# Optimization experiments

Measured on AMD Instinct MI355X. Metric: run time of the kernel, lower is better.

## Reference

```python
import jax, jax.numpy as jnp
import numpy as np

T, B, M, K, N = 8, 1, 16384, 128, 1024


def setup_inputs() -> dict:
    key = jax.random.key(0)
    k1, k2, k3 = jax.random.split(key, 3)
    inputs = jax.random.normal(k1, (T, B, M, K), dtype=jnp.float32)
    weights = jax.random.normal(k2, (T, B, K, N), dtype=jnp.float32) * (1.0 / np.sqrt(K))
    biases = jax.random.normal(k3, (T, 1, 1, N), dtype=jnp.float32)
    return {"inputs": inputs, "weights": weights, "biases": biases}


def reference(inputs, weights, biases):
    # FusedCombineBmm.forward with 3D per-group inputs:
    #   stack -> bmm over T*B -> view [T,B,M,N] -> + stacked bias -> gelu
    # inputs: [T,B,M,K], weights: [T,B,K,N], biases: [T,1,1,N]
    out = jnp.einsum('tbmk,tbkn->tbmn', inputs, weights)
    out = out + biases  # broadcast per-expert bias over (B, M)
    # act == 'gelu' (exact erf form, matching torch's default gelu)
    return jax.nn.gelu(out, approximate=False)
```

## Files before the change

kernel.cpp:

```cpp
#include <hip/hip_runtime.h>

#define T_DIM 8
#define M_DIM 16384
#define K_DIM 128
#define N_DIM 1024

typedef __attribute__((ext_vector_type(8))) short bf16x8_t;
typedef __attribute__((ext_vector_type(4))) float f32x4_t;

__device__ __forceinline__ unsigned short f2bf(float f) {
  unsigned int v;
  __builtin_memcpy(&v, &f, 4);
  v += 0x7FFFu + ((v >> 16) & 1u);
  return (unsigned short)(v >> 16);
}

__device__ __forceinline__ float gelu_tanh(float x) {
  float xc = fminf(fmaxf(x, -8.f), 8.f);
  float y = 2.3022144f * __builtin_fmaf(0.044715f * xc * xc, xc, xc);
  float t = __builtin_amdgcn_exp2f(y);
  return x * t * __builtin_amdgcn_rcpf(t + 1.0f);
}

__global__ __launch_bounds__(256) void transpose_w(
    const float* __restrict__ W, unsigned short* __restrict__ WT) {
  __shared__ __align__(16) unsigned short tile[64][72];
  int b = blockIdx.x;
  int t = b >> 5;
  int r = b & 31;
  int kt = r >> 4;
  int nt = r & 15;
  int tid = threadIdx.x;
  const float* src =
      W + (size_t)t * (K_DIM * N_DIM) + (size_t)(kt * 64) * N_DIM + nt * 64;
#pragma unroll
  for (int it = 0; it < 4; ++it) {
    int li = it * 256 + tid;
    int k = li >> 4;
    int c = li & 15;
    float4 v = *(const float4*)(src + (size_t)k * N_DIM + c * 4);
    unsigned short u[4] = {f2bf(v.x), f2bf(v.y), f2bf(v.z), f2bf(v.w)};
    *(uint2*)&tile[k][c * 4] = *(const uint2*)u;
  }
  __syncthreads();
  unsigned short* dst =
      WT + (size_t)t * (N_DIM * K_DIM) + (size_t)(nt * 64) * K_DIM + kt * 64;
#pragma unroll
  for (int it = 0; it < 2; ++it) {
    int li = it * 256 + tid;
    int n = li >> 3;
    int ck = li & 7;
    __align__(16) unsigned short tmp[8];
#pragma unroll
    for (int j = 0; j < 8; ++j) tmp[j] = tile[ck * 8 + j][n];
    *(uint4*)(dst + (size_t)n * K_DIM + ck * 8) = *(const uint4*)tmp;
  }
}

__global__ __launch_bounds__(256, 3) void gemm_bias_gelu(
    const float* __restrict__ A,
    const unsigned short* __restrict__ WT,
    const float* __restrict__ bias,
    float* __restrict__ O) {
  constexpr int BM = 64;
  constexpr int LDT = 136;
  __shared__ __align__(16) unsigned short sA[BM * LDT];

  int bid = blockIdx.x;
  int t = bid >> 8;
  int mt = bid & 255;
  int tid = threadIdx.x;
  int lane = tid & 63;
  int wn = tid >> 6;
  int qk = lane >> 4;
  int lr = lane & 15;

  const float* Ag =
      A + (size_t)t * ((size_t)M_DIM * K_DIM) + (size_t)(mt * BM) * K_DIM;
#pragma unroll
  for (int it = 0; it < 8; ++it) {
    int li = it * 256 + tid;
    int row = li >> 5;
    int c = li & 31;
    float4 va = *(const float4*)(Ag + (size_t)row * K_DIM + c * 4);
    unsigned short u[4] = {f2bf(va.x), f2bf(va.y), f2bf(va.z), f2bf(va.w)};
    *(uint2*)&sA[row * LDT + c * 4] = *(const uint2*)u;
  }
  __syncthreads();

  const unsigned short* Bg = WT + (size_t)t * (N_DIM * K_DIM);
  const float* bg = bias + t * N_DIM;
  float* Og = O + (size_t)t * ((size_t)M_DIM * N_DIM) +
              (size_t)(mt * BM) * N_DIM;

#pragma unroll 1
  for (int nb = 0; nb < 8; ++nb) {
    int n0 = nb * 128 + wn * 32;

    bf16x8_t bf[2][4];
#pragma unroll
    for (int j = 0; j < 2; ++j)
#pragma unroll
      for (int kk = 0; kk < 4; ++kk)
        bf[j][kk] = *(const bf16x8_t*)(Bg + (size_t)(n0 + j * 16 + lr) * K_DIM +
                                       kk * 32 + qk * 8);

    f32x4_t acc[4][2];
#pragma unroll
    for (int i = 0; i < 4; ++i)
#pragma unroll
      for (int j = 0; j < 2; ++j) acc[i][j] = (f32x4_t){0.f, 0.f, 0.f, 0.f};

#pragma unroll
    for (int kk = 0; kk < 4; ++kk) {
      bf16x8_t af[4];
#pragma unroll
      for (int i = 0; i < 4; ++i)
        af[i] = *(const bf16x8_t*)&sA[(i * 16 + lr) * LDT + kk * 32 + qk * 8];
#pragma unroll
      for (int i = 0; i < 4; ++i)
#pragma unroll
        for (int j = 0; j < 2; ++j)
          acc[i][j] = __builtin_amdgcn_mfma_f32_16x16x32_bf16(bf[j][kk], af[i],
                                                              acc[i][j], 0, 0, 0);
    }

#pragma unroll
    for (int j = 0; j < 2; ++j) {
      f32x4_t bv = *(const f32x4_t*)(bg + n0 + j * 16 + qk * 4);
#pragma unroll
      for (int i = 0; i < 4; ++i) {
        f32x4_t o;
#pragma unroll
        for (int rr = 0; rr < 4; ++rr) o[rr] = gelu_tanh(acc[i][j][rr] + bv[rr]);
        __builtin_nontemporal_store(
            o, (f32x4_t*)(Og + (size_t)(i * 16 + lr) * N_DIM + n0 + j * 16 +
                          qk * 4));
      }
    }
  }
}

extern "C" void kernel_launch(void* const* d_in, const int* in_sizes, int n_in,
                              void* d_out, int out_size, void* d_ws, size_t ws_size,
                              hipStream_t stream) {
  const float* A = (const float*)d_in[0];
  const float* W = (const float*)d_in[1];
  const float* bias = (const float*)d_in[2];
  float* O = (float*)d_out;
  unsigned short* WT = (unsigned short*)d_ws;

  transpose_w<<<256, 256, 0, stream>>>(W, WT);
  gemm_bias_gelu<<<2048, 256, 0, stream>>>(A, WT, bias, O);
}
```

Before: 658.5 us.

## Retile GEMM to 16-row blocks and stage output through LDS for contiguous stores

Each block now computes a 16x1024 output tile with 512 threads. Each wave covers 128 columns via eight 16x16 MFMA tiles, and the A fragments are loaded once into registers. The GELU results are written to a 64KB LDS buffer and then stored to global memory as fully contiguous row segments. The aim is to make the output writes, which dominate this memory-bound kernel, fully coalesced. In exchange, the weight matrix is reread four times as often per output row, each block adds a barrier, and the large LDS footprint limits occupancy.

```diff
diff --git a/kernel.cpp b/kernel.cpp
--- a/kernel.cpp
+++ b/kernel.cpp
@@ -57,18 +57,19 @@
   }
 }
 
-__global__ __launch_bounds__(256, 3) void gemm_bias_gelu(
+__global__ __launch_bounds__(512, 4) void gemm_bias_gelu(
     const float* __restrict__ A,
     const unsigned short* __restrict__ WT,
     const float* __restrict__ bias,
     float* __restrict__ O) {
-  constexpr int BM = 64;
   constexpr int LDT = 136;
-  __shared__ __align__(16) unsigned short sA[BM * LDT];
+  constexpr int LDO = 1028;
+  __shared__ __align__(16) unsigned short sA[16 * LDT];
+  __shared__ __align__(16) float sO[16 * LDO];
 
   int bid = blockIdx.x;
-  int t = bid >> 8;
-  int mt = bid & 255;
+  int t = bid >> 10;
+  int mt = bid & 1023;
   int tid = threadIdx.x;
   int lane = tid & 63;
   int wn = tid >> 6;
@@ -76,68 +77,63 @@
   int lr = lane & 15;
 
   const float* Ag =
-      A + (size_t)t * ((size_t)M_DIM * K_DIM) + (size_t)(mt * BM) * K_DIM;
-#pragma unroll
-  for (int it = 0; it < 8; ++it) {
-    int li = it * 256 + tid;
-    int row = li >> 5;
-    int c = li & 31;
+      A + (size_t)t * ((size_t)M_DIM * K_DIM) + (size_t)(mt * 16) * K_DIM;
+  {
+    int row = tid >> 5;
+    int c = tid & 31;
     float4 va = *(const float4*)(Ag + (size_t)row * K_DIM + c * 4);
     unsigned short u[4] = {f2bf(va.x), f2bf(va.y), f2bf(va.z), f2bf(va.w)};
     *(uint2*)&sA[row * LDT + c * 4] = *(const uint2*)u;
   }
   __syncthreads();
 
+  bf16x8_t af[4];
+#pragma unroll
+  for (int kk = 0; kk < 4; ++kk)
+    af[kk] = *(const bf16x8_t*)&sA[lr * LDT + kk * 32 + qk * 8];
+
   const unsigned short* Bg = WT + (size_t)t * (N_DIM * K_DIM);
-  const float* bg = bias + t * N_DIM;
-  float* Og = O + (size_t)t * ((size_t)M_DIM * N_DIM) +
-              (size_t)(mt * BM) * N_DIM;
 
-#pragma unroll 1
-  for (int nb = 0; nb < 8; ++nb) {
-    int n0 = nb * 128 + wn * 32;
-
-    bf16x8_t bf[2][4];
+  f32x4_t acc[8];
 #pragma unroll
-    for (int j = 0; j < 2; ++j)
-#pragma unroll
-      for (int kk = 0; kk < 4; ++kk)
-        bf[j][kk] = *(const bf16x8_t*)(Bg + (size_t)(n0 + j * 16 + lr) * K_DIM +
-                                       kk * 32 + qk * 8);
-
-    f32x4_t acc[4][2];
-#pragma unroll
-    for (int i = 0; i < 4; ++i)
-#pragma unroll
-      for (int j = 0; j < 2; ++j) acc[i][j] = (f32x4_t){0.f, 0.f, 0.f, 0.f};
+  for (int i = 0; i < 8; ++i) acc[i] = (f32x4_t){0.f, 0.f, 0.f, 0.f};
 
 #pragma unroll
-    for (int kk = 0; kk < 4; ++kk) {
-      bf16x8_t af[4];
+  for (int nt8 = 0; nt8 < 8; ++nt8) {
+    const unsigned short* bp =
+        Bg + (size_t)(wn * 128 + nt8 * 16 + lr) * K_DIM + qk * 8;
+    bf16x8_t b0 = *(const bf16x8_t*)(bp);
+    bf16x8_t b1 = *(const bf16x8_t*)(bp + 32);
+    bf16x8_t b2 = *(const bf16x8_t*)(bp + 64);
+    bf16x8_t b3 = *(const bf16x8_t*)(bp + 96);
+    acc[nt8] = __builtin_amdgcn_mfma_f32_16x16x32_bf16(b0, af[0], acc[nt8], 0, 0, 0);
+    acc[nt8] = __builtin_amdgcn_mfma_f32_16x16x32_bf16(b1, af[1], acc[nt8], 0, 0, 0);
+    acc[nt8] = __builtin_amdgcn_mfma_f32_16x16x32_bf16(b2, af[2], acc[nt8], 0, 0, 0);
+    acc[nt8] = __builtin_amdgcn_mfma_f32_16x16x32_bf16(b3, af[3], acc[nt8], 0, 0, 0);
+  }
+
+  const float* bg = bias + t * N_DIM;
 #pragma unroll
-      for (int i = 0; i < 4; ++i)
-        af[i] = *(const bf16x8_t*)&sA[(i * 16 + lr) * LDT + kk * 32 + qk * 8];
+  for (int nt8 = 0; nt8 < 8; ++nt8) {
+    int n0 = wn * 128 + nt8 * 16 + qk * 4;
+    f32x4_t bv = *(const f32x4_t*)(bg + n0);
+    f32x4_t o;
 #pragma unroll
-      for (int i = 0; i < 4; ++i)
+    for (int rr = 0; rr < 4; ++rr) o[rr] = gelu_tanh(acc[nt8][rr] + bv[rr]);
+    *(f32x4_t*)&sO[lr * LDO + n0] = o;
+  }
+  __syncthreads();
+
+  float* Og = O + (size_t)t * ((size_t)M_DIM * N_DIM) +
+              (size_t)(mt * 16) * N_DIM;
 #pragma unroll
-        for (int j = 0; j < 2; ++j)
-          acc[i][j] = __builtin_amdgcn_mfma_f32_16x16x32_bf16(bf[j][kk], af[i],
-                                                              acc[i][j], 0, 0, 0);
-    }
-
-#pragma unroll
-    for (int j = 0; j < 2; ++j) {
-      f32x4_t bv = *(const f32x4_t*)(bg + n0 + j * 16 + qk * 4);
-#pragma unroll
-      for (int i = 0; i < 4; ++i) {
-        f32x4_t o;
-#pragma unroll
-        for (int rr = 0; rr < 4; ++rr) o[rr] = gelu_tanh(acc[i][j][rr] + bv[rr]);
-        __builtin_nontemporal_store(
-            o, (f32x4_t*)(Og + (size_t)(i * 16 + lr) * N_DIM + n0 + j * 16 +
-                          qk * 4));
-      }
-    }
+  for (int p = 0; p < 8; ++p) {
+    int idx = p * 512 + tid;
+    int row = idx >> 8;
+    int cc = idx & 255;
+    f32x4_t v = *(const f32x4_t*)&sO[row * LDO + cc * 4];
+    __builtin_nontemporal_store(
+        v, (f32x4_t*)(Og + (size_t)row * N_DIM + cc * 4));
   }
 }
 
@@ -151,5 +147,5 @@
   unsigned short* WT = (unsigned short*)d_ws;
 
   transpose_w<<<256, 256, 0, stream>>>(W, WT);
-  gemm_bias_gelu<<<2048, 256, 0, stream>>>(A, WT, bias, O);
+  gemm_bias_gelu<<<8192, 512, 0, stream>>>(A, WT, bias, O);
 }
```

Result: slower. 731.6 us (+11.1%).

## Stage GELU output through double-buffered LDS for coalesced row stores

Applied to the files above, without the earlier changes.

Hoists the A fragments out of LDS into registers once, so the shared buffer can be reused for output staging. The N loop now covers 64-column chunks; results are written to a double-buffered LDS tile and then stored as contiguous 256-byte row segments rather than the scattered 16-lane MFMA output pattern. Occupancy is raised to 4 blocks per SM. The cost is a __syncthreads per chunk, higher register pressure from holding af[4][4], and less B reuse per chunk.

```diff
diff --git a/kernel.cpp b/kernel.cpp
--- a/kernel.cpp
+++ b/kernel.cpp
@@ -57,14 +57,15 @@
   }
 }
 
-__global__ __launch_bounds__(256, 3) void gemm_bias_gelu(
+__global__ __launch_bounds__(256, 4) void gemm_bias_gelu(
     const float* __restrict__ A,
     const unsigned short* __restrict__ WT,
     const float* __restrict__ bias,
     float* __restrict__ O) {
-  constexpr int BM = 64;
   constexpr int LDT = 136;
-  __shared__ __align__(16) unsigned short sA[BM * LDT];
+  constexpr int LDO = 68;
+  __shared__ __align__(16) unsigned char smem[2 * 64 * LDO * 4];
+  unsigned short* sA = (unsigned short*)smem;
 
   int bid = blockIdx.x;
   int t = bid >> 8;
@@ -76,7 +77,7 @@
   int lr = lane & 15;
 
   const float* Ag =
-      A + (size_t)t * ((size_t)M_DIM * K_DIM) + (size_t)(mt * BM) * K_DIM;
+      A + (size_t)t * ((size_t)M_DIM * K_DIM) + (size_t)(mt * 64) * K_DIM;
 #pragma unroll
   for (int it = 0; it < 8; ++it) {
     int li = it * 256 + tid;
@@ -88,55 +89,58 @@
   }
   __syncthreads();
 
+  bf16x8_t af[4][4];
+#pragma unroll
+  for (int i = 0; i < 4; ++i)
+#pragma unroll
+    for (int kk = 0; kk < 4; ++kk)
+      af[i][kk] = *(const bf16x8_t*)&sA[(i * 16 + lr) * LDT + kk * 32 + qk * 8];
+  __syncthreads();
+
   const unsigned short* Bg = WT + (size_t)t * (N_DIM * K_DIM);
   const float* bg = bias + t * N_DIM;
   float* Og = O + (size_t)t * ((size_t)M_DIM * N_DIM) +
-              (size_t)(mt * BM) * N_DIM;
+              (size_t)(mt * 64) * N_DIM;
 
 #pragma unroll 1
-  for (int nb = 0; nb < 8; ++nb) {
-    int n0 = nb * 128 + wn * 32;
+  for (int c = 0; c < 16; ++c) {
+    const unsigned short* bp =
+        Bg + (size_t)(c * 64 + wn * 16 + lr) * K_DIM + qk * 8;
+    bf16x8_t bf0 = *(const bf16x8_t*)(bp);
+    bf16x8_t bf1 = *(const bf16x8_t*)(bp + 32);
+    bf16x8_t bf2 = *(const bf16x8_t*)(bp + 64);
+    bf16x8_t bf3 = *(const bf16x8_t*)(bp + 96);
 
-    bf16x8_t bf[2][4];
+    f32x4_t acc[4];
 #pragma unroll
-    for (int j = 0; j < 2; ++j)
+    for (int i = 0; i < 4; ++i) acc[i] = (f32x4_t){0.f, 0.f, 0.f, 0.f};
 #pragma unroll
-      for (int kk = 0; kk < 4; ++kk)
-        bf[j][kk] = *(const bf16x8_t*)(Bg + (size_t)(n0 + j * 16 + lr) * K_DIM +
-                                       kk * 32 + qk * 8);
+    for (int i = 0; i < 4; ++i) {
+      acc[i] = __builtin_amdgcn_mfma_f32_16x16x32_bf16(bf0, af[i][0], acc[i], 0, 0, 0);
+      acc[i] = __builtin_amdgcn_mfma_f32_16x16x32_bf16(bf1, af[i][1], acc[i], 0, 0, 0);
+      acc[i] = __builtin_amdgcn_mfma_f32_16x16x32_bf16(bf2, af[i][2], acc[i], 0, 0, 0);
+      acc[i] = __builtin_amdgcn_mfma_f32_16x16x32_bf16(bf3, af[i][3], acc[i], 0, 0, 0);
+    }
 
-    f32x4_t acc[4][2];
+    float* sO = (float*)(smem + (c & 1) * (64 * LDO * 4));
+    f32x4_t bv = *(const f32x4_t*)(bg + c * 64 + wn * 16 + qk * 4);
 #pragma unroll
-    for (int i = 0; i < 4; ++i)
+    for (int i = 0; i < 4; ++i) {
+      f32x4_t o;
 #pragma unroll
-      for (int j = 0; j < 2; ++j) acc[i][j] = (f32x4_t){0.f, 0.f, 0.f, 0.f};
+      for (int rr = 0; rr < 4; ++rr) o[rr] = gelu_tanh(acc[i][rr] + bv[rr]);
+      *(f32x4_t*)&sO[(i * 16 + lr) * LDO + wn * 16 + qk * 4] = o;
+    }
+    __syncthreads();
 
 #pragma unroll
-    for (int kk = 0; kk < 4; ++kk) {
-      bf16x8_t af[4];
-#pragma unroll
-      for (int i = 0; i < 4; ++i)
-        af[i] = *(const bf16x8_t*)&sA[(i * 16 + lr) * LDT + kk * 32 + qk * 8];
-#pragma unroll
-      for (int i = 0; i < 4; ++i)
-#pragma unroll
-        for (int j = 0; j < 2; ++j)
-          acc[i][j] = __builtin_amdgcn_mfma_f32_16x16x32_bf16(bf[j][kk], af[i],
-                                                              acc[i][j], 0, 0, 0);
-    }
-
-#pragma unroll
-    for (int j = 0; j < 2; ++j) {
-      f32x4_t bv = *(const f32x4_t*)(bg + n0 + j * 16 + qk * 4);
-#pragma unroll
-      for (int i = 0; i < 4; ++i) {
-        f32x4_t o;
-#pragma unroll
-        for (int rr = 0; rr < 4; ++rr) o[rr] = gelu_tanh(acc[i][j][rr] + bv[rr]);
-        __builtin_nontemporal_store(
-            o, (f32x4_t*)(Og + (size_t)(i * 16 + lr) * N_DIM + n0 + j * 16 +
-                          qk * 4));
-      }
+    for (int p = 0; p < 4; ++p) {
+      int idx = p * 256 + tid;
+      int row = idx >> 4;
+      int cc = idx & 15;
+      f32x4_t v = *(const f32x4_t*)&sO[row * LDO + cc * 4];
+      __builtin_nontemporal_store(
+          v, (f32x4_t*)(Og + (size_t)row * N_DIM + c * 64 + cc * 4));
     }
   }
 }
```

New measurement: 612.9 us. -6.9%, faster.
